# Kernel optimization log

Hardware: AMD Instinct MI355X
Metric: run time of the kernel (lower is better)

The kernel has to match this reference:

```python
import jax, jax.numpy as jnp
import numpy as np

NUM_HEADS = 4   # num_heads init kwarg
KERNEL = 7      # kernel_size init kwarg
EPS = 1e-5      # nn.LayerNorm default eps


def setup_inputs() -> dict:
    key = jax.random.key(0)
    ks = jax.random.split(key, 6)
    C, depth = 128, 2
    x = jax.random.normal(ks[0], (2, C, 64, 64), jnp.float32)
    qkv_w = jax.random.normal(ks[1], (depth, 3 * C, C), jnp.float32) * 0.05
    qkv_b = jnp.zeros((depth, 3 * C), jnp.float32)
    rpb = jax.random.normal(ks[2], (depth, NUM_HEADS, 2 * KERNEL - 1, 2 * KERNEL - 1), jnp.float32) * 0.02
    proj_w = jax.random.normal(ks[3], (depth, C, C), jnp.float32) * 0.05
    proj_b = jnp.zeros((depth, C), jnp.float32)
    ln_g = jnp.ones((C,), jnp.float32)
    ln_b = jnp.zeros((C,), jnp.float32)
    return dict(x=x, qkv_w=qkv_w, qkv_b=qkv_b, rpb=rpb,
                proj_w=proj_w, proj_b=proj_b, ln_g=ln_g, ln_b=ln_b)


def _na2d(x, w_qkv, b_qkv, rpb, w_p, b_p):
    """NATTEN-style 2D neighborhood attention. x: (B,H,W,C)."""
    B, H, W, C = x.shape
    h, k = NUM_HEADS, KERNEL
    d = C // h
    qkv = (x @ w_qkv.T + b_qkv).reshape(B, H, W, 3, h, d)
    q = qkv[..., 0, :, :] * (d ** -0.5)   # (B,H,W,h,d)
    kk = qkv[..., 1, :, :]
    v = qkv[..., 2, :, :]
    # edge-clamped window starts: each query sees exactly k x k neighbors
    si = jnp.clip(jnp.arange(H) - k // 2, 0, H - k)
    sj = jnp.clip(jnp.arange(W) - k // 2, 0, W - k)
    idx_i = si[:, None] + jnp.arange(k)   # (H,k) absolute row indices
    idx_j = sj[:, None] + jnp.arange(k)   # (W,k) absolute col indices

    def win(t):  # (B,H,W,h,d) -> (B,H,W,k,k,h,d)
        t = t[:, idx_i]          # (B,H,k,W,h,d)
        t = t[:, :, :, idx_j]    # (B,H,k,W,k,h,d)
        return jnp.transpose(t, (0, 1, 3, 2, 4, 5, 6))

    kw = win(kk)
    vw = win(v)
    attn = jnp.einsum('bijhd,bijpqhd->bijhpq', q, kw)  # (B,H,W,h,k,k)
    # relative position bias: index = (neighbor_abs - query) + (k-1)
    bi = jnp.arange(k)[None, :] + (k - 1) - (jnp.arange(H) - si)[:, None]  # (H,k)
    bj = jnp.arange(k)[None, :] + (k - 1) - (jnp.arange(W) - sj)[:, None]  # (W,k)
    bias = rpb[:, bi[:, None, :, None], bj[None, :, None, :]]  # (h,H,W,k,k)
    attn = attn + jnp.transpose(bias, (1, 2, 0, 3, 4))[None]
    attn = jax.nn.softmax(attn.reshape(B, H, W, h, k * k), axis=-1).reshape(B, H, W, h, k, k)
    out = jnp.einsum('bijhpq,bijpqhd->bijhd', attn, vw).reshape(B, H, W, C)
    return out @ w_p.T + b_p


def reference(x, qkv_w, qkv_b, rpb, proj_w, proj_b, ln_g, ln_b):
    y = jnp.transpose(x, (0, 2, 3, 1))  # NCHW -> NHWC
    for l in range(qkv_w.shape[0]):     # depth=2 stacked NA layers
        y = _na2d(y, qkv_w[l], qkv_b[l], rpb[l], proj_w[l], proj_b[l])
    mu = y.mean(-1, keepdims=True)
    var = y.var(-1, keepdims=True)
    y = (y - mu) / jnp.sqrt(var + EPS) * ln_g + ln_b
    return jnp.transpose(y, (0, 3, 1, 2))  # NHWC -> NCHW
```

## Files before the change

kernel.cpp:

```cpp
#include <hip/hip_runtime.h>
#include <hip/hip_bf16.h>
#include <math.h>

#define PIX 8192
typedef __hip_bfloat16 bf16;
typedef __attribute__((ext_vector_type(8))) short short8;
typedef __attribute__((ext_vector_type(4))) float f32x4;

__device__ inline float bflo(unsigned u) { return __uint_as_float(u << 16); }
__device__ inline float bfhi(unsigned u) { return __uint_as_float(u & 0xffff0000u); }
__device__ inline unsigned short f2b(float f) {
  __hip_bfloat16 h = __float2bfloat16(f);
  return *reinterpret_cast<unsigned short*>(&h);
}
__device__ inline unsigned pack2(float a, float b) {
  return (unsigned)f2b(a) | ((unsigned)f2b(b) << 16);
}

__global__ __launch_bounds__(256) void cvtw(const float* __restrict__ qw,
                                            const float* __restrict__ pw,
                                            unsigned short* __restrict__ wq,
                                            unsigned short* __restrict__ wp) {
  int idx = blockIdx.x * 256 + threadIdx.x;
  if (idx < 98304) wq[idx] = f2b(qw[idx]);
  if (idx < 32768) wp[idx] = f2b(pw[idx]);
}

__global__ __launch_bounds__(256) void xqkv(const float* __restrict__ x,
                                            const unsigned short* __restrict__ wq,
                                            const float* __restrict__ qb,
                                            unsigned short* __restrict__ qkv) {
  __shared__ __align__(16) unsigned short As[16 * 136];
  int m0 = blockIdx.x * 16;
  int tid = threadIdx.x;
  int b = m0 >> 12, i = (m0 >> 6) & 63, j0 = m0 & 63;

  for (int idx = tid; idx < 2048; idx += 256) {
    int c = idx >> 4, jl = idx & 15;
    As[jl * 136 + c] =
        f2b(x[(size_t)b * 524288 + (size_t)c * 4096 + i * 64 + j0 + jl]);
  }
  __syncthreads();

  int w = tid >> 6, lane = tid & 63;
  int quad = lane >> 4, l16 = lane & 15;
  short8 a[4];
#pragma unroll
  for (int kc = 0; kc < 4; ++kc)
    a[kc] = *(const short8*)(As + l16 * 136 + kc * 32 + quad * 8);
#pragma unroll
  for (int nt = 0; nt < 6; ++nt) {
    int col = w * 96 + nt * 16 + l16;
    const short8* bp = (const short8*)(wq + (size_t)col * 128 + quad * 8);
    f32x4 c = {0.f, 0.f, 0.f, 0.f};
#pragma unroll
    for (int kc = 0; kc < 4; ++kc)
      c = __builtin_amdgcn_mfma_f32_16x16x32_bf16(a[kc], bp[kc * 4], c, 0, 0, 0);
    float bv = qb[col];
#pragma unroll
    for (int r2 = 0; r2 < 4; ++r2)
      qkv[(size_t)(m0 + quad * 4 + r2) * 384 + col] = f2b(c[r2] + bv);
  }
}

__global__ __launch_bounds__(256) void gemm_mfma(const unsigned short* __restrict__ A,
                                                 const unsigned short* __restrict__ W,
                                                 const float* __restrict__ bias,
                                                 unsigned short* __restrict__ Cmat,
                                                 int N) {
  int m0 = blockIdx.x * 64, n0 = blockIdx.y * 64;
  int tid = threadIdx.x;
  int w = tid >> 6, lane = tid & 63;
  int quad = lane >> 4, l16 = lane & 15;

  const short8* ap =
      (const short8*)(A + (size_t)(m0 + w * 16 + l16) * 128 + quad * 8);
  short8 a[4];
#pragma unroll
  for (int kc = 0; kc < 4; ++kc) a[kc] = ap[kc * 4];

  f32x4 acc[4];
#pragma unroll
  for (int nt = 0; nt < 4; ++nt) {
    const short8* bp =
        (const short8*)(W + (size_t)(n0 + nt * 16 + l16) * 128 + quad * 8);
    f32x4 c = {0.f, 0.f, 0.f, 0.f};
#pragma unroll
    for (int kc = 0; kc < 4; ++kc)
      c = __builtin_amdgcn_mfma_f32_16x16x32_bf16(a[kc], bp[kc * 4], c, 0, 0, 0);
    acc[nt] = c;
  }

#pragma unroll
  for (int nt = 0; nt < 4; ++nt) {
    int col = n0 + nt * 16 + l16;
    float bv = bias[col];
#pragma unroll
    for (int r = 0; r < 4; ++r) {
      int m = m0 + w * 16 + quad * 4 + r;
      Cmat[(size_t)m * N + col] = f2b(acc[nt][r] + bv);
    }
  }
}

#define RSTRIDE 72
__global__ __launch_bounds__(256, 2) void na_attn(const unsigned short* __restrict__ qkvp,
                                                  const float* __restrict__ rpb,
                                                  unsigned short* __restrict__ out) {
  __shared__ __align__(16) unsigned short kbuf[140 * RSTRIDE];
  __shared__ __align__(16) unsigned short vbuf[140 * RSTRIDE];
  __shared__ float rb[338];
  __shared__ float sc[64][52];

  int ti = blockIdx.x >> 4, tj = blockIdx.x & 15;
  int hp = blockIdx.y;
  int bz = blockIdx.z;
  int tid = threadIdx.x;
  int bi0 = ti * 8 - 3, bj0 = tj * 4 - 3;

  for (int t = tid; t < 338; t += 256) rb[t] = rpb[hp * 338 + t];

  for (int t = tid; t < 2240; t += 256) {
    int row = t >> 4;
    int sub = t & 15;
    int isv = sub >> 3;
    int c = sub & 7;
    int ri = row / 10, rj = row - ri * 10;
    int gi = bi0 + ri, gj = bj0 + rj;
    uint4 val = make_uint4(0, 0, 0, 0);
    if ((unsigned)gi < 64u && (unsigned)gj < 64u) {
      int pixn = (bz * 64 + gi) * 64 + gj;
      val = *(const uint4*)(qkvp + (size_t)pixn * 384 + 128 + isv * 128 +
                            hp * 64 + c * 8);
    }
    *(uint4*)((isv ? vbuf : kbuf) + row * RSTRIDE + c * 8) = val;
  }
  __syncthreads();

  int r = tid & 3;
  int hl = (tid >> 2) & 1;
  int px = tid >> 3;
  int ph = px * 2 + hl;
  int pi = px >> 2, pj = px & 3;
  int i = ti * 8 + pi, j = tj * 4 + pj;
  int si = min(max(i - 3, 0), 57), sj = min(max(j - 3, 0), 57);
  int li = si - bi0, lj = sj - bj0;
  int oi = i - si, oj = j - sj;
  int H = hp * 2 + hl;
  int pix = (bz * 64 + i) * 64 + j;

  const float scale = 0.17677669529663687f;
  float q[8];
  {
    uint4 t = *(const uint4*)(qkvp + (size_t)pix * 384 + H * 32 + r * 8);
    q[0] = bflo(t.x) * scale;  q[1] = bfhi(t.x) * scale;
    q[2] = bflo(t.y) * scale;  q[3] = bfhi(t.y) * scale;
    q[4] = bflo(t.z) * scale;  q[5] = bfhi(t.z) * scale;
    q[6] = bflo(t.w) * scale;  q[7] = bfhi(t.w) * scale;
  }

  const unsigned short* kh = kbuf + hl * 32 + r * 8;
  const unsigned short* vh = vbuf + hl * 32 + r * 8;
  const float* rbh = rb + hl * 169;

#pragma unroll
  for (int p = 0; p < 7; ++p) {
#pragma unroll
    for (int qq = 0; qq < 7; ++qq) {
      int n = (li + p) * 10 + (lj + qq);
      uint4 t = *(const uint4*)(kh + n * RSTRIDE);
      float dot = q[0] * bflo(t.x) + q[1] * bfhi(t.x)
                + q[2] * bflo(t.y) + q[3] * bfhi(t.y)
                + q[4] * bflo(t.z) + q[5] * bfhi(t.z)
                + q[6] * bflo(t.w) + q[7] * bfhi(t.w);
      dot += __shfl_xor(dot, 1);
      dot += __shfl_xor(dot, 2);
      if (r == 0) sc[ph][p * 7 + qq] = dot + rbh[(p + 6 - oi) * 13 + (qq + 6 - oj)];
    }
  }
  __syncthreads();

  float m = -INFINITY;
#pragma unroll
  for (int n = 0; n < 49; ++n) m = fmaxf(m, sc[ph][n]);

  float sum = 0.f;
  float acc[8] = {0.f, 0.f, 0.f, 0.f, 0.f, 0.f, 0.f, 0.f};
#pragma unroll
  for (int p = 0; p < 7; ++p) {
#pragma unroll
    for (int qq = 0; qq < 7; ++qq) {
      float e = __expf(sc[ph][p * 7 + qq] - m);
      sum += e;
      int n = (li + p) * 10 + (lj + qq);
      uint4 t = *(const uint4*)(vh + n * RSTRIDE);
      acc[0] += e * bflo(t.x);  acc[1] += e * bfhi(t.x);
      acc[2] += e * bflo(t.y);  acc[3] += e * bfhi(t.y);
      acc[4] += e * bflo(t.z);  acc[5] += e * bfhi(t.z);
      acc[6] += e * bflo(t.w);  acc[7] += e * bfhi(t.w);
    }
  }
  float inv = 1.f / sum;
  uint4 t;
  t.x = pack2(acc[0] * inv, acc[1] * inv);
  t.y = pack2(acc[2] * inv, acc[3] * inv);
  t.z = pack2(acc[4] * inv, acc[5] * inv);
  t.w = pack2(acc[6] * inv, acc[7] * inv);
  *(uint4*)(out + (size_t)pix * 128 + H * 32 + r * 8) = t;
}

__global__ __launch_bounds__(256) void ln_out(const unsigned short* __restrict__ y,
                                              const float* __restrict__ g,
                                              const float* __restrict__ bta,
                                              float* __restrict__ out) {
  __shared__ float tile[64][129];
  __shared__ float mean_s[64], rstd_s[64];
  int blk = blockIdx.x;
  int b = blk >> 6, i = blk & 63;
  int tid = threadIdx.x;
  const unsigned short* yrow = y + (size_t)blk * 64 * 128;
  for (int idx = tid; idx < 8192; idx += 256) {
    int j = idx >> 7, c = idx & 127;
    tile[j][c] = __uint_as_float((unsigned)yrow[idx] << 16);
  }
  __syncthreads();
  int jj = tid >> 2, qtr = tid & 3;
  float sum = 0.f, sumsq = 0.f;
#pragma unroll
  for (int cc = 0; cc < 32; ++cc) {
    float v = tile[jj][qtr * 32 + cc];
    sum += v; sumsq += v * v;
  }
  sum += __shfl_xor(sum, 1);  sum += __shfl_xor(sum, 2);
  sumsq += __shfl_xor(sumsq, 1);  sumsq += __shfl_xor(sumsq, 2);
  if (qtr == 0) {
    float mu = sum * (1.f / 128.f);
    mean_s[jj] = mu;
    rstd_s[jj] = rsqrtf(sumsq * (1.f / 128.f) - mu * mu + 1e-5f);
  }
  __syncthreads();
  int c0 = tid >> 6;
  int j = tid & 63;
  for (int c = c0; c < 128; c += 4) {
    float v = (tile[j][c] - mean_s[j]) * rstd_s[j] * g[c] + bta[c];
    out[(((size_t)b * 128 + c) * 64 + i) * 64 + j] = v;
  }
}

extern "C" void kernel_launch(void* const* d_in, const int* in_sizes, int n_in,
                              void* d_out, int out_size, void* d_ws, size_t ws_size,
                              hipStream_t stream) {
  (void)in_sizes; (void)n_in; (void)out_size; (void)ws_size;
  const float* x   = (const float*)d_in[0];
  const float* qw  = (const float*)d_in[1];
  const float* qb  = (const float*)d_in[2];
  const float* rpb = (const float*)d_in[3];
  const float* pw  = (const float*)d_in[4];
  const float* pb  = (const float*)d_in[5];
  const float* lg  = (const float*)d_in[6];
  const float* lb  = (const float*)d_in[7];

  unsigned short* y    = (unsigned short*)d_ws;
  unsigned short* qkv  = y + (size_t)PIX * 128;
  unsigned short* wq   = qkv + (size_t)PIX * 384;
  unsigned short* wp   = wq + 98304;
  unsigned short* attn = (unsigned short*)d_out;
  float* out = (float*)d_out;

  cvtw<<<384, 256, 0, stream>>>(qw, pw, wq, wp);
  xqkv<<<512, 256, 0, stream>>>(x, wq, qb, qkv);
  na_attn<<<dim3(128, 2, 2), 256, 0, stream>>>(qkv, rpb, attn);
  gemm_mfma<<<dim3(128, 2), 256, 0, stream>>>(attn, wp, pb, y, 128);
  gemm_mfma<<<dim3(128, 6), 256, 0, stream>>>(y, wq + 49152, qb + 384, qkv, 384);
  na_attn<<<dim3(128, 2, 2), 256, 0, stream>>>(qkv, rpb + 676, attn);
  gemm_mfma<<<dim3(128, 2), 256, 0, stream>>>(attn, wp + 16384, pb + 128, y, 128);
  ln_out<<<128, 256, 0, stream>>>(y, lg, lb, out);
}
```

Measured before the change: 146.3 us.

## Drop weight-conversion kernel and fuse final projection with LayerNorm

Removes the separate fp32-to-bf16 weight conversion launch: the GEMM kernels now read fp32 weights directly and convert them to bf16 in registers before the MFMA. The last projection GEMM and the LayerNorm output kernel are merged into one kernel that keeps the projected tile in shared memory, which saves a launch and a bf16 round-trip of y through global memory. In exchange every block reads twice as many weight bytes and repeats the conversion, and the fused kernel runs only 128 blocks, each doing a full 128-column GEMM.

```diff
diff --git a/kernel.cpp b/kernel.cpp
--- a/kernel.cpp
+++ b/kernel.cpp
@@ -16,18 +16,19 @@
 __device__ inline unsigned pack2(float a, float b) {
   return (unsigned)f2b(a) | ((unsigned)f2b(b) << 16);
 }
-
-__global__ __launch_bounds__(256) void cvtw(const float* __restrict__ qw,
-                                            const float* __restrict__ pw,
-                                            unsigned short* __restrict__ wq,
-                                            unsigned short* __restrict__ wp) {
-  int idx = blockIdx.x * 256 + threadIdx.x;
-  if (idx < 98304) wq[idx] = f2b(qw[idx]);
-  if (idx < 32768) wp[idx] = f2b(pw[idx]);
+__device__ inline short8 ldw8(const float* __restrict__ p) {
+  f32x4 lo = *(const f32x4*)p;
+  f32x4 hi = *(const f32x4*)(p + 4);
+  short8 r;
+  r[0] = (short)f2b(lo[0]); r[1] = (short)f2b(lo[1]);
+  r[2] = (short)f2b(lo[2]); r[3] = (short)f2b(lo[3]);
+  r[4] = (short)f2b(hi[0]); r[5] = (short)f2b(hi[1]);
+  r[6] = (short)f2b(hi[2]); r[7] = (short)f2b(hi[3]);
+  return r;
 }
 
 __global__ __launch_bounds__(256) void xqkv(const float* __restrict__ x,
-                                            const unsigned short* __restrict__ wq,
+                                            const float* __restrict__ qw,
                                             const float* __restrict__ qb,
                                             unsigned short* __restrict__ qkv) {
   __shared__ __align__(16) unsigned short As[16 * 136];
@@ -51,11 +52,11 @@
 #pragma unroll
   for (int nt = 0; nt < 6; ++nt) {
     int col = w * 96 + nt * 16 + l16;
-    const short8* bp = (const short8*)(wq + (size_t)col * 128 + quad * 8);
+    const float* wrow = qw + (size_t)col * 128 + quad * 8;
     f32x4 c = {0.f, 0.f, 0.f, 0.f};
 #pragma unroll
     for (int kc = 0; kc < 4; ++kc)
-      c = __builtin_amdgcn_mfma_f32_16x16x32_bf16(a[kc], bp[kc * 4], c, 0, 0, 0);
+      c = __builtin_amdgcn_mfma_f32_16x16x32_bf16(a[kc], ldw8(wrow + kc * 32), c, 0, 0, 0);
     float bv = qb[col];
 #pragma unroll
     for (int r2 = 0; r2 < 4; ++r2)
@@ -64,7 +65,7 @@
 }
 
 __global__ __launch_bounds__(256) void gemm_mfma(const unsigned short* __restrict__ A,
-                                                 const unsigned short* __restrict__ W,
+                                                 const float* __restrict__ Wf,
                                                  const float* __restrict__ bias,
                                                  unsigned short* __restrict__ Cmat,
                                                  int N) {
@@ -82,12 +83,11 @@
   f32x4 acc[4];
 #pragma unroll
   for (int nt = 0; nt < 4; ++nt) {
-    const short8* bp =
-        (const short8*)(W + (size_t)(n0 + nt * 16 + l16) * 128 + quad * 8);
+    const float* wrow = Wf + (size_t)(n0 + nt * 16 + l16) * 128 + quad * 8;
     f32x4 c = {0.f, 0.f, 0.f, 0.f};
 #pragma unroll
     for (int kc = 0; kc < 4; ++kc)
-      c = __builtin_amdgcn_mfma_f32_16x16x32_bf16(a[kc], bp[kc * 4], c, 0, 0, 0);
+      c = __builtin_amdgcn_mfma_f32_16x16x32_bf16(a[kc], ldw8(wrow + kc * 32), c, 0, 0, 0);
     acc[nt] = c;
   }
 
@@ -209,7 +209,9 @@
   *(uint4*)(out + (size_t)pix * 128 + H * 32 + r * 8) = t;
 }
 
-__global__ __launch_bounds__(256) void ln_out(const unsigned short* __restrict__ y,
+__global__ __launch_bounds__(256) void projln(const unsigned short* __restrict__ A,
+                                              const float* __restrict__ Wf,
+                                              const float* __restrict__ bias,
                                               const float* __restrict__ g,
                                               const float* __restrict__ bta,
                                               float* __restrict__ out) {
@@ -217,13 +219,32 @@
   __shared__ float mean_s[64], rstd_s[64];
   int blk = blockIdx.x;
   int b = blk >> 6, i = blk & 63;
-  int tid = threadIdx.x;
-  const unsigned short* yrow = y + (size_t)blk * 64 * 128;
-  for (int idx = tid; idx < 8192; idx += 256) {
-    int j = idx >> 7, c = idx & 127;
-    tile[j][c] = __uint_as_float((unsigned)yrow[idx] << 16);
-  }
-  __syncthreads();
+  int m0 = blk * 64;
+  int tid = threadIdx.x;
+  int w = tid >> 6, lane = tid & 63;
+  int quad = lane >> 4, l16 = lane & 15;
+
+  const short8* ap =
+      (const short8*)(A + (size_t)(m0 + w * 16 + l16) * 128 + quad * 8);
+  short8 a[4];
+#pragma unroll
+  for (int kc = 0; kc < 4; ++kc) a[kc] = ap[kc * 4];
+
+#pragma unroll
+  for (int nt = 0; nt < 8; ++nt) {
+    int col = nt * 16 + l16;
+    const float* wrow = Wf + (size_t)col * 128 + quad * 8;
+    f32x4 c = {0.f, 0.f, 0.f, 0.f};
+#pragma unroll
+    for (int kc = 0; kc < 4; ++kc)
+      c = __builtin_amdgcn_mfma_f32_16x16x32_bf16(a[kc], ldw8(wrow + kc * 32), c, 0, 0, 0);
+    float bv = bias[col];
+#pragma unroll
+    for (int r = 0; r < 4; ++r)
+      tile[w * 16 + quad * 4 + r][col] = c[r] + bv;
+  }
+  __syncthreads();
+
   int jj = tid >> 2, qtr = tid & 3;
   float sum = 0.f, sumsq = 0.f;
 #pragma unroll
@@ -262,17 +283,13 @@
 
   unsigned short* y    = (unsigned short*)d_ws;
   unsigned short* qkv  = y + (size_t)PIX * 128;
-  unsigned short* wq   = qkv + (size_t)PIX * 384;
-  unsigned short* wp   = wq + 98304;
-  unsigned short* attn = (unsigned short*)d_out;
+  unsigned short* attn = qkv + (size_t)PIX * 384;
   float* out = (float*)d_out;
 
-  cvtw<<<384, 256, 0, stream>>>(qw, pw, wq, wp);
-  xqkv<<<512, 256, 0, stream>>>(x, wq, qb, qkv);
+  xqkv<<<512, 256, 0, stream>>>(x, qw, qb, qkv);
   na_attn<<<dim3(128, 2, 2), 256, 0, stream>>>(qkv, rpb, attn);
-  gemm_mfma<<<dim3(128, 2), 256, 0, stream>>>(attn, wp, pb, y, 128);
-  gemm_mfma<<<dim3(128, 6), 256, 0, stream>>>(y, wq + 49152, qb + 384, qkv, 384);
+  gemm_mfma<<<dim3(128, 2), 256, 0, stream>>>(attn, pw, pb, y, 128);
+  gemm_mfma<<<dim3(128, 6), 256, 0, stream>>>(y, qw + 49152, qb + 384, qkv, 384);
   na_attn<<<dim3(128, 2, 2), 256, 0, stream>>>(qkv, rpb + 676, attn);
-  gemm_mfma<<<dim3(128, 2), 256, 0, stream>>>(attn, wp + 16384, pb + 128, y, 128);
-  ln_out<<<128, 256, 0, stream>>>(y, lg, lb, out);
-}
+  projln<<<128, 256, 0, stream>>>(attn, pw + 16384, pb + 128, lg, lb, out);
+}
```

Result: slower. 158.4 us (+8.3%).
